# Optimization experiments

Hardware: AMD Instinct MI355X
Metric: run time of the kernel (lower is better)

The kernel has to match this reference:

```python
import jax, jax.numpy as jnp
import numpy as np
from jax import lax

B = 16384
BN_EPS = 1e-5


def setup_inputs() -> dict:
    key = jax.random.key(0)
    ks = jax.random.split(key, 6)
    x = jax.random.normal(ks[0], (B, 1, 28, 28), jnp.float32)
    conv_w = jax.random.normal(ks[1], (4, 1, 3, 3), jnp.float32) * 0.2
    bn_gamma = jnp.ones((4,), jnp.float32)
    bn_beta = jnp.zeros((4,), jnp.float32)
    bn_mean = jnp.zeros((4,), jnp.float32)
    bn_var = jnp.ones((4,), jnp.float32)
    var_params = jax.random.normal(ks[2], (4,), jnp.float32)
    lin_w = jax.random.normal(ks[3], (10, 784), jnp.float32) * 0.03
    lin_b = jnp.zeros((10,), jnp.float32)
    return {"x": x, "conv_w": conv_w, "bn_gamma": bn_gamma, "bn_beta": bn_beta,
            "bn_mean": bn_mean, "bn_var": bn_var, "var_params": var_params,
            "lin_w": lin_w, "lin_b": lin_b}


def _ry_w0(s, theta):
    # apply RY(theta) to wire 0 (axis -2) of real state s[..., 2, 2]
    c, si = jnp.cos(theta * 0.5), jnp.sin(theta * 0.5)
    R = jnp.stack([jnp.stack([c, -si]), jnp.stack([si, c])])
    return jnp.einsum('ij,...jk->...ik', R, s)


def _ry_w1(s, theta):
    # apply RY(theta) to wire 1 (axis -1)
    c, si = jnp.cos(theta * 0.5), jnp.sin(theta * 0.5)
    R = jnp.stack([jnp.stack([c, -si]), jnp.stack([si, c])])
    return jnp.einsum('ij,...kj->...ki', R, s)


def _quantum_features(img, v):
    # img: [B, 28, 28] -> features [B, 196*4] (patch-major, 4 expvals each)
    b = img.shape[0]
    p = img.reshape(b, 14, 2, 14, 2).transpose(0, 1, 3, 2, 4)  # [B,14,14,2,2]
    # encoding RYs on same wire compose: angles a = p0+p2 (wire0), b = p1+p3 (wire1)
    ha = (p[..., 0, 0] + p[..., 1, 0]) * 0.5
    hb = (p[..., 0, 1] + p[..., 1, 1]) * 0.5
    w0 = jnp.stack([jnp.cos(ha), jnp.sin(ha)], axis=-1)
    w1 = jnp.stack([jnp.cos(hb), jnp.sin(hb)], axis=-1)
    s = w0[..., :, None] * w1[..., None, :]  # real statevector [B,14,14,2,2]
    # CNOT(control=0, target=1): flip wire1 where wire0 == 1
    s = jnp.stack([s[..., 0, :], s[..., 1, ::-1]], axis=-2)
    s = _ry_w0(s, v[0])
    s = _ry_w1(s, v[1])
    # CNOT(control=1, target=0): flip wire0 where wire1 == 1
    s = jnp.stack([s[..., :, 0], s[..., ::-1, 1]], axis=-1)
    s = _ry_w0(s, v[2])
    s = _ry_w1(s, v[3])
    z0 = jnp.sum(s[..., 0, :] ** 2 - s[..., 1, :] ** 2, axis=-1)
    z1 = jnp.sum(s[..., :, 0] ** 2 - s[..., :, 1] ** 2, axis=-1)
    x0 = 2.0 * jnp.sum(s[..., 0, :] * s[..., 1, :], axis=-1)
    x1 = 2.0 * jnp.sum(s[..., :, 0] * s[..., :, 1], axis=-1)
    return jnp.stack([z0, z1, x0, x1], axis=-1).reshape(b, -1)  # [B,784]


def reference(x, conv_w, bn_gamma, bn_beta, bn_mean, bn_var, var_params, lin_w, lin_b):
    b = x.shape[0]
    # classical branch: conv(s=2,p=1) -> BN (eval) -> ReLU -> flatten
    h = lax.conv_general_dilated(x, conv_w, window_strides=(2, 2),
                                 padding=((1, 1), (1, 1)))  # [B,4,14,14]
    inv = bn_gamma / jnp.sqrt(bn_var + BN_EPS)
    h = h * inv[None, :, None, None] + (bn_beta - bn_mean * inv)[None, :, None, None]
    h = jnp.maximum(h, 0.0)
    cls_out = h.reshape(b, -1)  # [B,784]
    # quantum branch over 2x2 patches
    q_out = _quantum_features(x[:, 0], var_params)  # [B,784]
    fused = cls_out + q_out
    logits = fused @ lin_w.T + lin_b
    return jax.nn.log_softmax(logits, axis=-1)
```

## Files before the change

kernel.cpp:

```cpp
#include <hip/hip_runtime.h>
#include <math.h>


typedef __fp16 h2 __attribute__((ext_vector_type(2)));
typedef __fp16 h4 __attribute__((ext_vector_type(4)));
typedef __fp16 h8 __attribute__((ext_vector_type(8)));
typedef float f32x4 __attribute__((ext_vector_type(4)));

#define NSAMP 16
#define FSTRIDE 808

__global__ void quanv_precomp(const float* __restrict__ conv_w,
                              const float* __restrict__ bn_gamma,
                              const float* __restrict__ bn_beta,
                              const float* __restrict__ bn_mean,
                              const float* __restrict__ bn_var,
                              const float* __restrict__ var_params,
                              float* __restrict__ ws)
{
    if (threadIdx.x != 0 || blockIdx.x != 0) return;

    #pragma unroll
    for (int c = 0; c < 4; ++c) {
        float iv = bn_gamma[c] * rsqrtf(bn_var[c] + 1e-5f);
        #pragma unroll
        for (int k = 0; k < 9; ++k) ws[c * 9 + k] = conv_w[c * 9 + k] * iv;
        ws[36 + c] = bn_beta[c] - bn_mean[c] * iv;
    }

    float cv[4], sv[4];
    #pragma unroll
    for (int k = 0; k < 4; ++k) __sincosf(var_params[k] * 0.5f, &sv[k], &cv[k]);

    float U[4][4];
    #pragma unroll
    for (int col = 0; col < 4; ++col) {
        float v0 = (col == 0), v1 = (col == 1), v2 = (col == 2), v3 = (col == 3);
        float t;
        t = v2; v2 = v3; v3 = t;
        t = cv[0]*v0 - sv[0]*v2; v2 = sv[0]*v0 + cv[0]*v2; v0 = t;
        t = cv[0]*v1 - sv[0]*v3; v3 = sv[0]*v1 + cv[0]*v3; v1 = t;
        t = cv[1]*v0 - sv[1]*v1; v1 = sv[1]*v0 + cv[1]*v1; v0 = t;
        t = cv[1]*v2 - sv[1]*v3; v3 = sv[1]*v2 + cv[1]*v3; v2 = t;
        t = v1; v1 = v3; v3 = t;
        t = cv[2]*v0 - sv[2]*v2; v2 = sv[2]*v0 + cv[2]*v2; v0 = t;
        t = cv[2]*v1 - sv[2]*v3; v3 = sv[2]*v1 + cv[2]*v3; v1 = t;
        t = cv[3]*v0 - sv[3]*v1; v1 = sv[3]*v0 + cv[3]*v1; v0 = t;
        t = cv[3]*v2 - sv[3]*v3; v3 = sv[3]*v2 + cv[3]*v3; v2 = t;
        U[0][col] = v0; U[1][col] = v1; U[2][col] = v2; U[3][col] = v3;
    }

    #pragma unroll
    for (int f = 0; f < 4; ++f) {
        float M[4][4];
        #pragma unroll
        for (int r = 0; r < 4; ++r) {
            int src = r; float sgn = 1.f;
            if      (f == 0) { sgn = (r < 2) ? 1.f : -1.f; }
            else if (f == 1) { sgn = ((r & 1) == 0) ? 1.f : -1.f; }
            else if (f == 2) { src = r ^ 2; }
            else             { src = r ^ 1; }
            #pragma unroll
            for (int j = 0; j < 4; ++j) M[r][j] = sgn * U[src][j];
        }
        float A[4][4];
        #pragma unroll
        for (int i = 0; i < 4; ++i)
            #pragma unroll
            for (int j = 0; j < 4; ++j)
                A[i][j] = U[0][i]*M[0][j] + U[1][i]*M[1][j]
                        + U[2][i]*M[2][j] + U[3][i]*M[3][j];

        float a1 = 0.5f*(A[0][0]+A[1][1]), b1 = 0.5f*(A[0][0]-A[1][1]), g1 = 0.5f*(A[0][1]+A[1][0]);
        float a2 = 0.5f*(A[2][2]+A[3][3]), b2 = 0.5f*(A[2][2]-A[3][3]), g2 = 0.5f*(A[2][3]+A[3][2]);
        float u00 = A[0][2]+A[2][0], u01 = A[0][3]+A[2][1];
        float u10 = A[1][2]+A[3][0], u11 = A[1][3]+A[3][1];
        float a3 = 0.5f*(u00+u11), b3 = 0.5f*(u00-u11), g3 = 0.5f*(u01+u10);

        float* K = ws + 40 + 9 * f;
        K[0] = 0.5f*(a1+a2); K[1] = 0.5f*(a1-a2); K[2] = 0.5f*a3;
        K[3] = 0.5f*(b1+b2); K[4] = 0.5f*(b1-b2); K[5] = 0.5f*b3;
        K[6] = 0.5f*(g1+g2); K[7] = 0.5f*(g1-g2); K[8] = 0.5f*g3;
    }
}

__global__ __launch_bounds__(256, 3)
void quanv_main(const float* __restrict__ x,
                const float* __restrict__ ws,
                const float* __restrict__ lin_w,
                const float* __restrict__ lin_b,
                float* __restrict__ out, int B)
{
    __shared__ __align__(16) __fp16 clsB[NSAMP * FSTRIDE];
    __shared__ __align__(16) __fp16 qB[NSAMP * FSTRIDE];

    const int tid  = threadIdx.x;
    const int lane = tid & 63;
    const int wave = tid >> 6;

    {
        int r = tid >> 4, buf = (tid >> 3) & 1, w = tid & 7;
        int* wp = (int*)((buf ? qB : clsB) + r * FSTRIDE + 784);
        wp[w] = 0;
    }

    const int bcol = lane & 15, bkg = lane >> 4;
    const __fp16 hz = (__fp16)0.f;
    h8 bfrag[7];
    #pragma unroll
    for (int t = 0; t < 7; ++t) {
        int st = wave * 7 + t;
        int kb = st * 32 + bkg * 8;
        h8 bf = {hz, hz, hz, hz, hz, hz, hz, hz};
        if (bcol < 10 && kb < 784) {
            const float4* lw4 = (const float4*)(lin_w + bcol * 784 + kb);
            float4 v0 = lw4[0], v1 = lw4[1];
            h2 p0 = __builtin_amdgcn_cvt_pkrtz(v0.x, v0.y);
            h2 p1 = __builtin_amdgcn_cvt_pkrtz(v0.z, v0.w);
            h2 p2 = __builtin_amdgcn_cvt_pkrtz(v1.x, v1.y);
            h2 p3 = __builtin_amdgcn_cvt_pkrtz(v1.z, v1.w);
            h8 tv = {p0.x, p0.y, p1.x, p1.y, p2.x, p2.y, p3.x, p3.y};
            bf = tv;
        }
        bfrag[t] = bf;
    }

    const int s_loc = tid >> 4;
    const int pcol  = tid & 15;
    const int sg    = blockIdx.x * NSAMP + s_loc;
    const int sgc   = (sg < B) ? sg : (B - 1);
    const float* xs = x + (size_t)sgc * 784;
    __fp16* clsRow  = clsB + s_loc * FSTRIDE;
    __fp16* qRow    = qB   + s_loc * FSTRIDE;

    #pragma unroll
    for (int it = 0; it < 13; ++it) {
        int p = pcol + 16 * it;
        p = (p < 196) ? p : 195;
        unsigned ii = (unsigned)p / 14u;
        int j  = p - (int)ii * 14;
        int om = (int)ii * 56 + 2 * j;

        float2 Rm = *(const float2*)(xs + om);
        float2 Rb = *(const float2*)(xs + om + 28);
        int ot = om - 28;  ot  = (ot  > 0) ? ot  : 0;
        float2 Rt = *(const float2*)(xs + ot);
        int olt = om - 30; olt = (olt > 0) ? olt : 0;
        float2 Lt = *(const float2*)(xs + olt);
        int olm = om - 2;  olm = (olm > 0) ? olm : 0;
        float2 Lm = *(const float2*)(xs + olm);
        float2 Lb = *(const float2*)(xs + olm + 28);

        float mt = (ii > 0u) ? 1.f : 0.f;
        float ml = (j  > 0 ) ? 1.f : 0.f;
        float a00 = Lt.y * (mt * ml), a01 = Rt.x * mt, a02 = Rt.y * mt;
        float a10 = Lm.y * ml,        a11 = Rm.x,      a12 = Rm.y;
        float a20 = Lb.y * ml,        a21 = Rb.x,      a22 = Rb.y;

        #pragma unroll
        for (int c = 0; c < 4; ++c) {
            float h = ws[36 + c];
            h = fmaf(ws[c*9+0], a00, h); h = fmaf(ws[c*9+1], a01, h);
            h = fmaf(ws[c*9+2], a02, h); h = fmaf(ws[c*9+3], a10, h);
            h = fmaf(ws[c*9+4], a11, h); h = fmaf(ws[c*9+5], a12, h);
            h = fmaf(ws[c*9+6], a20, h); h = fmaf(ws[c*9+7], a21, h);
            h = fmaf(ws[c*9+8], a22, h);
            clsRow[c * 196 + p] = (__fp16)fmaxf(h, 0.f);
        }

        float cA, sA, cB, sB;
        __sincosf(a11 + a21, &sA, &cA);
        __sincosf(a12 + a22, &sB, &cB);
        float o[4];
        #pragma unroll
        for (int f = 0; f < 4; ++f) {
            const float* k = ws + 40 + 9 * f;
            float t1 = fmaf(k[2], sA, fmaf(k[1], cA, k[0]));
            float t2 = fmaf(k[5], sA, fmaf(k[4], cA, k[3]));
            float t3 = fmaf(k[8], sA, fmaf(k[7], cA, k[6]));
            o[f] = fmaf(t3, sB, fmaf(t2, cB, t1));
        }
        h2 zz = __builtin_amdgcn_cvt_pkrtz(o[0], o[1]);
        h2 xx = __builtin_amdgcn_cvt_pkrtz(o[2], o[3]);
        h4 qv = {zz.x, zz.y, xx.x, xx.y};
        *(h4*)(qRow + 4 * p) = qv;
    }

    __syncthreads();

    f32x4 acc = {0.f, 0.f, 0.f, 0.f};
    {
        const int arow = lane & 15, akg = lane >> 4;
        #pragma unroll
        for (int t = 0; t < 7; ++t) {
            int st = wave * 7 + t;
            if (st < 25) {
                int off = arow * FSTRIDE + st * 32 + akg * 8;
                h8 a = *(const h8*)(clsB + off) + *(const h8*)(qB + off);
                acc = __builtin_amdgcn_mfma_f32_16x16x32_f16(a, bfrag[t], acc, 0, 0, 0);
            }
        }
    }

    __syncthreads();
    float* pw = (float*)clsB;
    {
        const int col = lane & 15, rb = (lane >> 4) * 4;
        #pragma unroll
        for (int r = 0; r < 4; ++r)
            pw[(wave * 16 + rb + r) * 16 + col] = acc[r];
    }
    __syncthreads();

    {
        const int c = tid & 15;
        float L = pw[s_loc * 16 + c] + pw[(16 + s_loc) * 16 + c]
                + pw[(32 + s_loc) * 16 + c] + pw[(48 + s_loc) * 16 + c];
        L = (c < 10) ? (L + lin_b[c]) : -1e30f;
        float mx = L;
        mx = fmaxf(mx, __shfl_xor(mx, 1, 16));
        mx = fmaxf(mx, __shfl_xor(mx, 2, 16));
        mx = fmaxf(mx, __shfl_xor(mx, 4, 16));
        mx = fmaxf(mx, __shfl_xor(mx, 8, 16));
        float se = (c < 10) ? __expf(L - mx) : 0.f;
        se += __shfl_xor(se, 1, 16);
        se += __shfl_xor(se, 2, 16);
        se += __shfl_xor(se, 4, 16);
        se += __shfl_xor(se, 8, 16);
        if (c < 10 && sg < B)
            out[(size_t)sg * 10 + c] = L - mx - __logf(se);
    }
}

extern "C" void kernel_launch(void* const* d_in, const int* in_sizes, int n_in,
                              void* d_out, int out_size, void* d_ws, size_t ws_size,
                              hipStream_t stream) {
    const float* x          = (const float*)d_in[0];
    const float* conv_w     = (const float*)d_in[1];
    const float* bn_gamma   = (const float*)d_in[2];
    const float* bn_beta    = (const float*)d_in[3];
    const float* bn_mean    = (const float*)d_in[4];
    const float* bn_var     = (const float*)d_in[5];
    const float* var_params = (const float*)d_in[6];
    const float* lin_w      = (const float*)d_in[7];
    const float* lin_b      = (const float*)d_in[8];
    float* out = (float*)d_out;
    float* ws  = (float*)d_ws;

    const int B = in_sizes[0] / 784;
    quanv_precomp<<<1, 64, 0, stream>>>(conv_w, bn_gamma, bn_beta, bn_mean,
                                        bn_var, var_params, ws);
    const int blocks = (B + NSAMP - 1) / NSAMP;
    quanv_main<<<blocks, 256, 0, stream>>>(x, ws, lin_w, lin_b, out, B);
}
```

Baseline: 124.2 us.

## Fuse parameter precompute into main kernel and halve samples per block

Removes the single-thread precompute kernel and its workspace round trip. Each block now derives the BN scale/shift and the rotation sines and cosines itself and broadcasts them with readfirstlane. The quantum circuit is evaluated directly per patch instead of through a precomputed 9-coefficient form. Each block now handles 8 samples with 32 threads per sample and allows higher occupancy. The MFMA tiles are now half empty, and every block repeats the parameter setup and applies more per-patch arithmetic.

```diff
diff --git a/kernel.cpp b/kernel.cpp
--- a/kernel.cpp
+++ b/kernel.cpp
@@ -7,89 +7,24 @@
 typedef __fp16 h8 __attribute__((ext_vector_type(8)));
 typedef float f32x4 __attribute__((ext_vector_type(4)));
 
-#define NSAMP 16
+#define NSAMP 8
 #define FSTRIDE 808
 
-__global__ void quanv_precomp(const float* __restrict__ conv_w,
-                              const float* __restrict__ bn_gamma,
-                              const float* __restrict__ bn_beta,
-                              const float* __restrict__ bn_mean,
-                              const float* __restrict__ bn_var,
-                              const float* __restrict__ var_params,
-                              float* __restrict__ ws)
-{
-    if (threadIdx.x != 0 || blockIdx.x != 0) return;
-
-    #pragma unroll
-    for (int c = 0; c < 4; ++c) {
-        float iv = bn_gamma[c] * rsqrtf(bn_var[c] + 1e-5f);
-        #pragma unroll
-        for (int k = 0; k < 9; ++k) ws[c * 9 + k] = conv_w[c * 9 + k] * iv;
-        ws[36 + c] = bn_beta[c] - bn_mean[c] * iv;
-    }
-
-    float cv[4], sv[4];
-    #pragma unroll
-    for (int k = 0; k < 4; ++k) __sincosf(var_params[k] * 0.5f, &sv[k], &cv[k]);
-
-    float U[4][4];
-    #pragma unroll
-    for (int col = 0; col < 4; ++col) {
-        float v0 = (col == 0), v1 = (col == 1), v2 = (col == 2), v3 = (col == 3);
-        float t;
-        t = v2; v2 = v3; v3 = t;
-        t = cv[0]*v0 - sv[0]*v2; v2 = sv[0]*v0 + cv[0]*v2; v0 = t;
-        t = cv[0]*v1 - sv[0]*v3; v3 = sv[0]*v1 + cv[0]*v3; v1 = t;
-        t = cv[1]*v0 - sv[1]*v1; v1 = sv[1]*v0 + cv[1]*v1; v0 = t;
-        t = cv[1]*v2 - sv[1]*v3; v3 = sv[1]*v2 + cv[1]*v3; v2 = t;
-        t = v1; v1 = v3; v3 = t;
-        t = cv[2]*v0 - sv[2]*v2; v2 = sv[2]*v0 + cv[2]*v2; v0 = t;
-        t = cv[2]*v1 - sv[2]*v3; v3 = sv[2]*v1 + cv[2]*v3; v1 = t;
-        t = cv[3]*v0 - sv[3]*v1; v1 = sv[3]*v0 + cv[3]*v1; v0 = t;
-        t = cv[3]*v2 - sv[3]*v3; v3 = sv[3]*v2 + cv[3]*v3; v2 = t;
-        U[0][col] = v0; U[1][col] = v1; U[2][col] = v2; U[3][col] = v3;
-    }
-
-    #pragma unroll
-    for (int f = 0; f < 4; ++f) {
-        float M[4][4];
-        #pragma unroll
-        for (int r = 0; r < 4; ++r) {
-            int src = r; float sgn = 1.f;
-            if      (f == 0) { sgn = (r < 2) ? 1.f : -1.f; }
-            else if (f == 1) { sgn = ((r & 1) == 0) ? 1.f : -1.f; }
-            else if (f == 2) { src = r ^ 2; }
-            else             { src = r ^ 1; }
-            #pragma unroll
-            for (int j = 0; j < 4; ++j) M[r][j] = sgn * U[src][j];
-        }
-        float A[4][4];
-        #pragma unroll
-        for (int i = 0; i < 4; ++i)
-            #pragma unroll
-            for (int j = 0; j < 4; ++j)
-                A[i][j] = U[0][i]*M[0][j] + U[1][i]*M[1][j]
-                        + U[2][i]*M[2][j] + U[3][i]*M[3][j];
-
-        float a1 = 0.5f*(A[0][0]+A[1][1]), b1 = 0.5f*(A[0][0]-A[1][1]), g1 = 0.5f*(A[0][1]+A[1][0]);
-        float a2 = 0.5f*(A[2][2]+A[3][3]), b2 = 0.5f*(A[2][2]-A[3][3]), g2 = 0.5f*(A[2][3]+A[3][2]);
-        float u00 = A[0][2]+A[2][0], u01 = A[0][3]+A[2][1];
-        float u10 = A[1][2]+A[3][0], u11 = A[1][3]+A[3][1];
-        float a3 = 0.5f*(u00+u11), b3 = 0.5f*(u00-u11), g3 = 0.5f*(u01+u10);
-
-        float* K = ws + 40 + 9 * f;
-        K[0] = 0.5f*(a1+a2); K[1] = 0.5f*(a1-a2); K[2] = 0.5f*a3;
-        K[3] = 0.5f*(b1+b2); K[4] = 0.5f*(b1-b2); K[5] = 0.5f*b3;
-        K[6] = 0.5f*(g1+g2); K[7] = 0.5f*(g1-g2); K[8] = 0.5f*g3;
-    }
+__device__ __forceinline__ float rfl(float v) {
+    return __int_as_float(__builtin_amdgcn_readfirstlane(__float_as_int(v)));
 }
 
-__global__ __launch_bounds__(256, 3)
-void quanv_main(const float* __restrict__ x,
-                const float* __restrict__ ws,
-                const float* __restrict__ lin_w,
-                const float* __restrict__ lin_b,
-                float* __restrict__ out, int B)
+__global__ __launch_bounds__(256, 6)
+void quanv_fused(const float* __restrict__ x,
+                 const float* __restrict__ conv_w,
+                 const float* __restrict__ bn_gamma,
+                 const float* __restrict__ bn_beta,
+                 const float* __restrict__ bn_mean,
+                 const float* __restrict__ bn_var,
+                 const float* __restrict__ var_params,
+                 const float* __restrict__ lin_w,
+                 const float* __restrict__ lin_b,
+                 float* __restrict__ out, int B)
 {
     __shared__ __align__(16) __fp16 clsB[NSAMP * FSTRIDE];
     __shared__ __align__(16) __fp16 qB[NSAMP * FSTRIDE];
@@ -98,7 +33,7 @@
     const int lane = tid & 63;
     const int wave = tid >> 6;
 
-    {
+    if (tid < 128) {
         int r = tid >> 4, buf = (tid >> 3) & 1, w = tid & 7;
         int* wp = (int*)((buf ? qB : clsB) + r * FSTRIDE + 784);
         wp[w] = 0;
@@ -106,12 +41,13 @@
 
     const int bcol = lane & 15, bkg = lane >> 4;
     const __fp16 hz = (__fp16)0.f;
+    const h8 hz8 = {hz, hz, hz, hz, hz, hz, hz, hz};
     h8 bfrag[7];
     #pragma unroll
     for (int t = 0; t < 7; ++t) {
         int st = wave * 7 + t;
         int kb = st * 32 + bkg * 8;
-        h8 bf = {hz, hz, hz, hz, hz, hz, hz, hz};
+        h8 bf = hz8;
         if (bcol < 10 && kb < 784) {
             const float4* lw4 = (const float4*)(lin_w + bcol * 784 + kb);
             float4 v0 = lw4[0], v1 = lw4[1];
@@ -125,8 +61,23 @@
         bfrag[t] = bf;
     }
 
-    const int s_loc = tid >> 4;
-    const int pcol  = tid & 15;
+    float inv[4], addc[4];
+    #pragma unroll
+    for (int c = 0; c < 4; ++c) {
+        float iv = bn_gamma[c] * rsqrtf(bn_var[c] + 1e-5f);
+        inv[c]  = rfl(iv);
+        addc[c] = rfl(bn_beta[c] - bn_mean[c] * iv);
+    }
+    float cv[4], sv[4];
+    #pragma unroll
+    for (int k = 0; k < 4; ++k) {
+        float s, c;
+        __sincosf(var_params[k] * 0.5f, &s, &c);
+        sv[k] = rfl(s); cv[k] = rfl(c);
+    }
+
+    const int s_loc = tid >> 5;
+    const int q32   = tid & 31;
     const int sg    = blockIdx.x * NSAMP + s_loc;
     const int sgc   = (sg < B) ? sg : (B - 1);
     const float* xs = x + (size_t)sgc * 784;
@@ -134,56 +85,64 @@
     __fp16* qRow    = qB   + s_loc * FSTRIDE;
 
     #pragma unroll
-    for (int it = 0; it < 13; ++it) {
-        int p = pcol + 16 * it;
-        p = (p < 196) ? p : 195;
-        unsigned ii = (unsigned)p / 14u;
-        int j  = p - (int)ii * 14;
-        int om = (int)ii * 56 + 2 * j;
-
-        float2 Rm = *(const float2*)(xs + om);
-        float2 Rb = *(const float2*)(xs + om + 28);
-        int ot = om - 28;  ot  = (ot  > 0) ? ot  : 0;
-        float2 Rt = *(const float2*)(xs + ot);
-        int olt = om - 30; olt = (olt > 0) ? olt : 0;
-        float2 Lt = *(const float2*)(xs + olt);
-        int olm = om - 2;  olm = (olm > 0) ? olm : 0;
-        float2 Lm = *(const float2*)(xs + olm);
-        float2 Lb = *(const float2*)(xs + olm + 28);
-
-        float mt = (ii > 0u) ? 1.f : 0.f;
-        float ml = (j  > 0 ) ? 1.f : 0.f;
-        float a00 = Lt.y * (mt * ml), a01 = Rt.x * mt, a02 = Rt.y * mt;
-        float a10 = Lm.y * ml,        a11 = Rm.x,      a12 = Rm.y;
-        float a20 = Lb.y * ml,        a21 = Rb.x,      a22 = Rb.y;
-
-        #pragma unroll
-        for (int c = 0; c < 4; ++c) {
-            float h = ws[36 + c];
-            h = fmaf(ws[c*9+0], a00, h); h = fmaf(ws[c*9+1], a01, h);
-            h = fmaf(ws[c*9+2], a02, h); h = fmaf(ws[c*9+3], a10, h);
-            h = fmaf(ws[c*9+4], a11, h); h = fmaf(ws[c*9+5], a12, h);
-            h = fmaf(ws[c*9+6], a20, h); h = fmaf(ws[c*9+7], a21, h);
-            h = fmaf(ws[c*9+8], a22, h);
-            clsRow[c * 196 + p] = (__fp16)fmaxf(h, 0.f);
+    for (int it = 0; it < 7; ++it) {
+        int p = q32 + 32 * it;
+        if (p < 196) {
+            unsigned ii = (unsigned)p / 14u;
+            int j  = p - (int)ii * 14;
+            int om = (int)ii * 56 + 2 * j;
+
+            float2 Rm = *(const float2*)(xs + om);
+            float2 Rb = *(const float2*)(xs + om + 28);
+            int ot = om - 28;  ot  = (ot  > 0) ? ot  : 0;
+            float2 Rt = *(const float2*)(xs + ot);
+            int olt = om - 30; olt = (olt > 0) ? olt : 0;
+            float2 Lt = *(const float2*)(xs + olt);
+            int olm = om - 2;  olm = (olm > 0) ? olm : 0;
+            float2 Lm = *(const float2*)(xs + olm);
+            float2 Lb = *(const float2*)(xs + olm + 28);
+
+            float mt = (ii > 0u) ? 1.f : 0.f;
+            float ml = (j  > 0 ) ? 1.f : 0.f;
+            float a00 = Lt.y * (mt * ml), a01 = Rt.x * mt, a02 = Rt.y * mt;
+            float a10 = Lm.y * ml,        a11 = Rm.x,      a12 = Rm.y;
+            float a20 = Lb.y * ml,        a21 = Rb.x,      a22 = Rb.y;
+
+            #pragma unroll
+            for (int c = 0; c < 4; ++c) {
+                float h = conv_w[c*9+0]*a00 + conv_w[c*9+1]*a01 + conv_w[c*9+2]*a02
+                        + conv_w[c*9+3]*a10 + conv_w[c*9+4]*a11 + conv_w[c*9+5]*a12
+                        + conv_w[c*9+6]*a20 + conv_w[c*9+7]*a21 + conv_w[c*9+8]*a22;
+                h = h * inv[c] + addc[c];
+                clsRow[c * 196 + p] = (__fp16)fmaxf(h, 0.f);
+            }
+
+            float ha = 0.5f * (a11 + a21);
+            float hb = 0.5f * (a12 + a22);
+            float c0, s0, c1, s1;
+            __sincosf(ha, &s0, &c0);
+            __sincosf(hb, &s1, &c1);
+            float m00 = c0*c1, m01 = c0*s1;
+            float m10 = s0*s1, m11 = s0*c1;
+            float t00 = cv[0]*m00 - sv[0]*m10, t01 = cv[0]*m01 - sv[0]*m11;
+            float t10 = sv[0]*m00 + cv[0]*m10, t11 = sv[0]*m01 + cv[0]*m11;
+            float u00 = cv[1]*t00 - sv[1]*t01, u01 = sv[1]*t00 + cv[1]*t01;
+            float u10 = cv[1]*t10 - sv[1]*t11, u11 = sv[1]*t10 + cv[1]*t11;
+            float tmp = u01; u01 = u11; u11 = tmp;
+            float p00 = cv[2]*u00 - sv[2]*u10, p01 = cv[2]*u01 - sv[2]*u11;
+            float p10 = sv[2]*u00 + cv[2]*u10, p11 = sv[2]*u01 + cv[2]*u11;
+            float q00 = cv[3]*p00 - sv[3]*p01, q01 = sv[3]*p00 + cv[3]*p01;
+            float q10 = cv[3]*p10 - sv[3]*p11, q11 = sv[3]*p10 + cv[3]*p11;
+
+            float z0 = q00*q00 + q01*q01 - q10*q10 - q11*q11;
+            float z1 = q00*q00 + q10*q10 - q01*q01 - q11*q11;
+            float x0 = 2.f * (q00*q10 + q01*q11);
+            float x1 = 2.f * (q00*q01 + q10*q11);
+            h2 zz = __builtin_amdgcn_cvt_pkrtz(z0, z1);
+            h2 xx = __builtin_amdgcn_cvt_pkrtz(x0, x1);
+            h4 qv = {zz.x, zz.y, xx.x, xx.y};
+            *(h4*)(qRow + 4 * p) = qv;
         }
-
-        float cA, sA, cB, sB;
-        __sincosf(a11 + a21, &sA, &cA);
-        __sincosf(a12 + a22, &sB, &cB);
-        float o[4];
-        #pragma unroll
-        for (int f = 0; f < 4; ++f) {
-            const float* k = ws + 40 + 9 * f;
-            float t1 = fmaf(k[2], sA, fmaf(k[1], cA, k[0]));
-            float t2 = fmaf(k[5], sA, fmaf(k[4], cA, k[3]));
-            float t3 = fmaf(k[8], sA, fmaf(k[7], cA, k[6]));
-            o[f] = fmaf(t3, sB, fmaf(t2, cB, t1));
-        }
-        h2 zz = __builtin_amdgcn_cvt_pkrtz(o[0], o[1]);
-        h2 xx = __builtin_amdgcn_cvt_pkrtz(o[2], o[3]);
-        h4 qv = {zz.x, zz.y, xx.x, xx.y};
-        *(h4*)(qRow + 4 * p) = qv;
     }
 
     __syncthreads();
@@ -195,8 +154,11 @@
         for (int t = 0; t < 7; ++t) {
             int st = wave * 7 + t;
             if (st < 25) {
-                int off = arow * FSTRIDE + st * 32 + akg * 8;
-                h8 a = *(const h8*)(clsB + off) + *(const h8*)(qB + off);
+                h8 a = hz8;
+                if (arow < NSAMP) {
+                    int off = arow * FSTRIDE + st * 32 + akg * 8;
+                    a = *(const h8*)(clsB + off) + *(const h8*)(qB + off);
+                }
                 acc = __builtin_amdgcn_mfma_f32_16x16x32_f16(a, bfrag[t], acc, 0, 0, 0);
             }
         }
@@ -204,18 +166,19 @@
 
     __syncthreads();
     float* pw = (float*)clsB;
-    {
+    if (lane < 32) {
         const int col = lane & 15, rb = (lane >> 4) * 4;
         #pragma unroll
         for (int r = 0; r < 4; ++r)
-            pw[(wave * 16 + rb + r) * 16 + col] = acc[r];
+            pw[(wave * 8 + rb + r) * 16 + col] = acc[r];
     }
     __syncthreads();
 
-    {
-        const int c = tid & 15;
-        float L = pw[s_loc * 16 + c] + pw[(16 + s_loc) * 16 + c]
-                + pw[(32 + s_loc) * 16 + c] + pw[(48 + s_loc) * 16 + c];
+    if (tid < 128) {
+        const int c  = tid & 15;
+        const int sl = tid >> 4;
+        float L = pw[sl * 16 + c] + pw[(8 + sl) * 16 + c]
+                + pw[(16 + sl) * 16 + c] + pw[(24 + sl) * 16 + c];
         L = (c < 10) ? (L + lin_b[c]) : -1e30f;
         float mx = L;
         mx = fmaxf(mx, __shfl_xor(mx, 1, 16));
@@ -227,8 +190,9 @@
         se += __shfl_xor(se, 2, 16);
         se += __shfl_xor(se, 4, 16);
         se += __shfl_xor(se, 8, 16);
-        if (c < 10 && sg < B)
-            out[(size_t)sg * 10 + c] = L - mx - __logf(se);
+        const int sg2 = blockIdx.x * NSAMP + sl;
+        if (c < 10 && sg2 < B)
+            out[(size_t)sg2 * 10 + c] = L - mx - __logf(se);
     }
 }
 
@@ -245,11 +209,9 @@
     const float* lin_w      = (const float*)d_in[7];
     const float* lin_b      = (const float*)d_in[8];
     float* out = (float*)d_out;
-    float* ws  = (float*)d_ws;
 
     const int B = in_sizes[0] / 784;
-    quanv_precomp<<<1, 64, 0, stream>>>(conv_w, bn_gamma, bn_beta, bn_mean,
-                                        bn_var, var_params, ws);
     const int blocks = (B + NSAMP - 1) / NSAMP;
-    quanv_main<<<blocks, 256, 0, stream>>>(x, ws, lin_w, lin_b, out, B);
+    quanv_fused<<<blocks, 256, 0, stream>>>(x, conv_w, bn_gamma, bn_beta, bn_mean,
+                                            bn_var, var_params, lin_w, lin_b, out, B);
 }
```

Result: faster. 110.8 us (-10.8%).
